# Kernel tuning notes

Hardware: AMD Instinct MI355X
Metric: run time of the kernel (lower is better)

## Reference

```python
import jax, jax.numpy as jnp
import numpy as np
from jax import lax

S, L = 8192, 16
N_WORD, N_CHAR = 50000, 128
WORD_DIM, CHAR_DIM = 256, 64
WORD_HID, CHAR_HID = 512, 128
N_TAG = 64


def _lstm_gates(x, h, Wih, Whh, bih, bhh):
    # x: [..., D], h: [..., H]; torch gate order: i, f, g, o
    g = x @ Wih.T + h @ Whh.T + bih + bhh
    i, f, gg, o = jnp.split(g, 4, axis=-1)
    return jax.nn.sigmoid(i), jax.nn.sigmoid(f), jnp.tanh(gg), jax.nn.sigmoid(o)


def setup_inputs() -> dict:
    key = jax.random.key(0)
    ks = jax.random.split(key, 16)
    sc = 0.1
    inp = {
        'x': jax.random.randint(ks[0], (S,), 0, N_WORD),
        'chars': jax.random.randint(ks[1], (S, L), 0, N_CHAR),
        'lengths': jax.random.randint(ks[2], (S,), 0, L),
        'word_emb': jax.random.normal(ks[3], (N_WORD, WORD_DIM), jnp.float32) * sc,
        'char_emb': jax.random.normal(ks[4], (N_CHAR, CHAR_DIM), jnp.float32) * sc,
        'c_Wih': jax.random.normal(ks[5], (4 * CHAR_HID, CHAR_DIM), jnp.float32) * sc,
        'c_Whh': jax.random.normal(ks[6], (4 * CHAR_HID, CHAR_HID), jnp.float32) * sc,
        'c_bih': jax.random.normal(ks[7], (4 * CHAR_HID,), jnp.float32) * sc,
        'c_bhh': jax.random.normal(ks[8], (4 * CHAR_HID,), jnp.float32) * sc,
        'w_Wih': jax.random.normal(ks[9], (4 * WORD_HID, WORD_DIM + CHAR_HID), jnp.float32) * sc,
        'w_Whh': jax.random.normal(ks[10], (4 * WORD_HID, WORD_HID), jnp.float32) * sc,
        'w_bih': jax.random.normal(ks[11], (4 * WORD_HID,), jnp.float32) * sc,
        'w_bhh': jax.random.normal(ks[12], (4 * WORD_HID,), jnp.float32) * sc,
        'lin_W': jax.random.normal(ks[13], (N_TAG, WORD_HID), jnp.float32) * sc,
        'lin_b': jax.random.normal(ks[14], (N_TAG,), jnp.float32) * sc,
    }
    return inp


def _char_features(chars, lengths, char_emb, Wih, Whh, bih, bhh):
    # batched char LSTM over all S words at once; returns final CELL state (h[1] in torch)
    emb = char_emb[chars]              # [S, L, char_dim]
    xs = jnp.swapaxes(emb, 0, 1)       # [L, S, char_dim]
    h0 = jnp.zeros((chars.shape[0], CHAR_HID), emb.dtype)
    c0 = jnp.zeros_like(h0)

    def step(carry, inp):
        h, c = carry
        x_t, t = inp
        i, f, g, o = _lstm_gates(x_t, h, Wih, Whh, bih, bhh)
        c_new = f * c + i * g
        h_new = o * jnp.tanh(c_new)
        m = (t < lengths)[:, None]     # only update within each word's true length
        return (jnp.where(m, h_new, h), jnp.where(m, c_new, c)), None

    (h, c), _ = lax.scan(step, (h0, c0), (xs, jnp.arange(L)))
    return c                            # [S, char_hidden]


def _word_lstm(seq, Wih, Whh, bih, bhh):
    # seq: [S, D] single sequence (batch=1 in original)
    h0 = jnp.zeros((WORD_HID,), seq.dtype)
    c0 = jnp.zeros_like(h0)

    def step(carry, x_t):
        h, c = carry
        i, f, g, o = _lstm_gates(x_t, h, Wih, Whh, bih, bhh)
        c = f * c + i * g
        h = o * jnp.tanh(c)
        return (h, c), h

    _, hs = lax.scan(step, (h0, c0), seq)
    return hs                           # [S, word_hidden]


def reference(x, chars, lengths, word_emb, char_emb,
              c_Wih, c_Whh, c_bih, c_bhh,
              w_Wih, w_Whh, w_bih, w_bhh,
              lin_W, lin_b):
    char_feat = _char_features(chars, lengths, char_emb, c_Wih, c_Whh, c_bih, c_bhh)
    we = word_emb[x]                                    # [S, word_dim]
    seq = jnp.concatenate([we, char_feat], axis=1)      # [S, word_dim+char_hidden]
    hs = _word_lstm(seq, w_Wih, w_Whh, w_bih, w_bhh)    # [S, word_hidden]
    logits = hs @ lin_W.T + lin_b                       # [S, n_tag]
    return jax.nn.log_softmax(logits, axis=1)
```

## Files before the change

kernel.cpp:

```cpp
#include <hip/hip_runtime.h>
#include <hip/hip_bf16.h>

#define S_LEN 8192
#define CLEN 16
#define WDIM 256
#define CDIM 64
#define CHID 128
#define WHID 512
#define GDIM 2048
#define NTAG 64
#define KDIM 384
#define NWG 32

typedef unsigned long long u64;

__device__ __forceinline__ float sigmoidf_(float x) {
  return 1.0f / (1.0f + __expf(-x));
}
__device__ __forceinline__ float tanhf_(float x) {
  return 1.0f - 2.0f / (__expf(2.0f * x) + 1.0f);
}

__global__ __launch_bounds__(256)
void char_lstm_kernel(const int* __restrict__ chars, const int* __restrict__ lengths,
                      const float* __restrict__ emb, const float* __restrict__ Wih,
                      const float* __restrict__ Whh, const float* __restrict__ bih,
                      const float* __restrict__ bhh, float* __restrict__ cf)
{
  __shared__ float xs[16][CDIM];
  __shared__ float hsm[16][CHID];
  __shared__ int cidx[16];
  __shared__ int lens[16];
  const int tid = threadIdx.x;
  const int grp = tid >> 7;
  const int j = tid & 127;
  const int wb = blockIdx.x * 16;

  for (int i = tid; i < 16 * CHID; i += 256) (&hsm[0][0])[i] = 0.f;
  if (tid < 16) lens[tid] = lengths[wb + tid];
  float c[8];
#pragma unroll
  for (int w = 0; w < 8; ++w) c[w] = 0.f;
  const float bi = bih[j] + bhh[j];
  const float bf = bih[CHID + j] + bhh[CHID + j];
  const float bg = bih[2 * CHID + j] + bhh[2 * CHID + j];
  const float bo = bih[3 * CHID + j] + bhh[3 * CHID + j];

  for (int t = 0; t < CLEN; ++t) {
    __syncthreads();
    if (tid < 16) cidx[tid] = chars[(wb + tid) * CLEN + t];
    __syncthreads();
    {
      int e = tid * 4;
      int wi = e >> 6;
      int k = e & 63;
      const float4 v = *(const float4*)(emb + (size_t)cidx[wi] * CDIM + k);
      *(float4*)(&xs[wi][k]) = v;
    }
    __syncthreads();
    float ai[8], af[8], ag[8], ao[8];
#pragma unroll
    for (int w = 0; w < 8; ++w) { ai[w] = bi; af[w] = bf; ag[w] = bg; ao[w] = bo; }
    for (int k = 0; k < CDIM; k += 4) {
      float4 w0 = *(const float4*)(Wih + (size_t)j * CDIM + k);
      float4 w1 = *(const float4*)(Wih + (size_t)(CHID + j) * CDIM + k);
      float4 w2 = *(const float4*)(Wih + (size_t)(2 * CHID + j) * CDIM + k);
      float4 w3 = *(const float4*)(Wih + (size_t)(3 * CHID + j) * CDIM + k);
#pragma unroll
      for (int s = 0; s < 4; ++s) {
        float wiv = (&w0.x)[s], wfv = (&w1.x)[s], wgv = (&w2.x)[s], wov = (&w3.x)[s];
#pragma unroll
        for (int w = 0; w < 8; ++w) {
          float xv = xs[grp * 8 + w][k + s];
          ai[w] = fmaf(wiv, xv, ai[w]);
          af[w] = fmaf(wfv, xv, af[w]);
          ag[w] = fmaf(wgv, xv, ag[w]);
          ao[w] = fmaf(wov, xv, ao[w]);
        }
      }
    }
    for (int k = 0; k < CHID; k += 4) {
      float4 w0 = *(const float4*)(Whh + (size_t)j * CHID + k);
      float4 w1 = *(const float4*)(Whh + (size_t)(CHID + j) * CHID + k);
      float4 w2 = *(const float4*)(Whh + (size_t)(2 * CHID + j) * CHID + k);
      float4 w3 = *(const float4*)(Whh + (size_t)(3 * CHID + j) * CHID + k);
#pragma unroll
      for (int s = 0; s < 4; ++s) {
        float wiv = (&w0.x)[s], wfv = (&w1.x)[s], wgv = (&w2.x)[s], wov = (&w3.x)[s];
#pragma unroll
        for (int w = 0; w < 8; ++w) {
          float hv = hsm[grp * 8 + w][k + s];
          ai[w] = fmaf(wiv, hv, ai[w]);
          af[w] = fmaf(wfv, hv, af[w]);
          ag[w] = fmaf(wgv, hv, ag[w]);
          ao[w] = fmaf(wov, hv, ao[w]);
        }
      }
    }
    __syncthreads();
#pragma unroll
    for (int w = 0; w < 8; ++w) {
      if (t < lens[grp * 8 + w]) {
        float iv = sigmoidf_(ai[w]);
        float fv = sigmoidf_(af[w]);
        float gv = tanhf_(ag[w]);
        float ov = sigmoidf_(ao[w]);
        c[w] = fv * c[w] + iv * gv;
        hsm[grp * 8 + w][j] = ov * tanhf_(c[w]);
      }
    }
  }
#pragma unroll
  for (int w = 0; w < 8; ++w)
    cf[(size_t)(wb + grp * 8 + w) * CHID + j] = c[w];
}

#define BM 64
#define BN 64
#define BK 32
__global__ __launch_bounds__(256)
void gx_gemm_kernel(const int* __restrict__ x, const float* __restrict__ word_emb,
                    const float* __restrict__ char_feat, const float* __restrict__ Wih,
                    const float* __restrict__ bih, const float* __restrict__ bhh,
                    float* __restrict__ Gx)
{
  __shared__ float As[BK][BM + 1];
  __shared__ float Bs[BK][BN + 1];
  __shared__ int xidx[BM];
  const int tid = threadIdx.x;
  const int tx = tid & 15, ty = tid >> 4;
  const int m0 = blockIdx.y * BM;
  const int n0 = blockIdx.x * BN;
  if (tid < BM) xidx[tid] = x[m0 + tid];
  float acc[4][4] = {};
  for (int k0 = 0; k0 < KDIM; k0 += BK) {
    __syncthreads();
    {
      int i = tid >> 5;
      int kk = tid & 31;
#pragma unroll
      for (int l = 0; l < 8; ++l) {
        int row = i + l * 8;
        int k = k0 + kk;
        int tt = m0 + row;
        float v = (k < WDIM) ? word_emb[(size_t)xidx[row] * WDIM + k]
                             : char_feat[(size_t)tt * CHID + (k - WDIM)];
        As[kk][row] = v;
      }
    }
    {
      int jjj = tid >> 5;
      int kk = tid & 31;
#pragma unroll
      for (int l = 0; l < 8; ++l) {
        int col = jjj + l * 8;
        Bs[kk][col] = Wih[(size_t)(n0 + col) * KDIM + k0 + kk];
      }
    }
    __syncthreads();
#pragma unroll
    for (int kk = 0; kk < BK; ++kk) {
      float a[4], b[4];
#pragma unroll
      for (int m = 0; m < 4; ++m) a[m] = As[kk][ty * 4 + m];
#pragma unroll
      for (int n = 0; n < 4; ++n) b[n] = Bs[kk][tx * 4 + n];
#pragma unroll
      for (int m = 0; m < 4; ++m)
#pragma unroll
        for (int n = 0; n < 4; ++n)
          acc[m][n] = fmaf(a[m], b[n], acc[m][n]);
    }
  }
#pragma unroll
  for (int n = 0; n < 4; ++n) {
    int g = n0 + tx * 4 + n;
    float bias = bih[g] + bhh[g];
#pragma unroll
    for (int m = 0; m < 4; ++m) {
      int tt = m0 + ty * 4 + m;
      Gx[(size_t)tt * GDIM + g] = acc[m][n] + bias;
    }
  }
}

__global__ __launch_bounds__(256, 1)
void word_lstm_seq(const float* __restrict__ Whh, const float* __restrict__ Gx,
                   float* __restrict__ hs, u64* hbuf)
{
  __shared__ float h_lds[WHID];
  __shared__ float red[2][256];
  const int tid = threadIdx.x;
  const int wg = blockIdx.x;
  const int cc = tid >> 6;
  const int lane = tid & 63;
  const int kb = cc * 128;

  const int grow = (lane >> 4) * WHID + wg * 16 + (lane & 15);
  float wl[128];
  {
    const float* wsrc = Whh + (size_t)grow * WHID + kb;
#pragma unroll
    for (int k = 0; k < 128; ++k) wl[k] = wsrc[k];
  }

  float c_state = 0.f;

  for (int t = 0; t < S_LEN; ++t) {
    float gxv = 0.f;
    if (tid < 64)
      gxv = Gx[(size_t)t * GDIM + grow];
    if (t > 0) {
      const u64* base = hbuf + (size_t)(t & 1) * WHID + kb;
      const int s0 = 2 * lane;
      u64 a, b;
      const unsigned want = (unsigned)t;
      while (true) {
        a = __hip_atomic_load(base + s0, __ATOMIC_RELAXED,
                              __HIP_MEMORY_SCOPE_AGENT);
        b = __hip_atomic_load(base + s0 + 1, __ATOMIC_RELAXED,
                              __HIP_MEMORY_SCOPE_AGENT);
        if ((unsigned)(a >> 32) == want && (unsigned)(b >> 32) == want) break;
      }
      float2 hv2 = make_float2(__uint_as_float((unsigned)a),
                               __uint_as_float((unsigned)b));
      *(float2*)(&h_lds[kb + s0]) = hv2;
    } else {
      *(float2*)(&h_lds[kb + 2 * lane]) = make_float2(0.f, 0.f);
    }
    __threadfence_block();
    float acc = 0.f;
#pragma unroll
    for (int g = 0; g < 32; ++g) {
      float4 hv = *(const float4*)(&h_lds[kb + 4 * g]);
      acc = fmaf(wl[4 * g + 0], hv.x, acc);
      acc = fmaf(wl[4 * g + 1], hv.y, acc);
      acc = fmaf(wl[4 * g + 2], hv.z, acc);
      acc = fmaf(wl[4 * g + 3], hv.w, acc);
    }
    red[t & 1][tid] = acc;
    __syncthreads();
    if (tid < 64) {
      const float* rp = &red[t & 1][0];
      float s = rp[tid] + rp[64 + tid] + rp[128 + tid] + rp[192 + tid] + gxv;
      float act = ((tid >> 4) == 2) ? tanhf_(s) : sigmoidf_(s);
      int jj = tid & 15;
      float iv = __shfl(act, jj);
      float fv = __shfl(act, 16 + jj);
      float gv = __shfl(act, 32 + jj);
      float ov = __shfl(act, 48 + jj);
      if (tid < 16) {
        c_state = fv * c_state + iv * gv;
        float hv = ov * tanhf_(c_state);
        const int hidx = wg * 16 + tid;
        u64 pkt = ((u64)(unsigned)(t + 1) << 32) | (u64)__float_as_uint(hv);
        (void)__hip_atomic_exchange(
            &hbuf[(size_t)((t + 1) & 1) * WHID + hidx], pkt,
            __ATOMIC_RELAXED, __HIP_MEMORY_SCOPE_AGENT);
        hs[(size_t)t * WHID + hidx] = hv;
      }
    }
  }
}

__global__ __launch_bounds__(256)
void tag_kernel(const float* __restrict__ hs, const float* __restrict__ W,
                const float* __restrict__ b, float* __restrict__ out)
{
  const int wave = threadIdx.x >> 6;
  const int lane = threadIdx.x & 63;
  const int t = blockIdx.x * 4 + wave;
  const float* hr = hs + (size_t)t * WHID;
  const float* wr = W + (size_t)lane * WHID;
  float acc = b[lane];
  for (int k = 0; k < WHID; k += 4) {
    float4 wv = *(const float4*)(wr + k);
    float4 hv = *(const float4*)(hr + k);
    acc = fmaf(wv.x, hv.x, acc);
    acc = fmaf(wv.y, hv.y, acc);
    acc = fmaf(wv.z, hv.z, acc);
    acc = fmaf(wv.w, hv.w, acc);
  }
  float m = acc;
#pragma unroll
  for (int off = 32; off > 0; off >>= 1) m = fmaxf(m, __shfl_xor(m, off));
  float e = __expf(acc - m);
  float sum = e;
#pragma unroll
  for (int off = 32; off > 0; off >>= 1) sum += __shfl_xor(sum, off);
  out[(size_t)t * NTAG + lane] = (acc - m) - __logf(sum);
}

extern "C" void kernel_launch(void* const* d_in, const int* in_sizes, int n_in,
                              void* d_out, int out_size, void* d_ws, size_t ws_size,
                              hipStream_t stream)
{
  const int* x          = (const int*)d_in[0];
  const int* chars      = (const int*)d_in[1];
  const int* lengths    = (const int*)d_in[2];
  const float* word_emb = (const float*)d_in[3];
  const float* char_emb = (const float*)d_in[4];
  const float* c_Wih    = (const float*)d_in[5];
  const float* c_Whh    = (const float*)d_in[6];
  const float* c_bih    = (const float*)d_in[7];
  const float* c_bhh    = (const float*)d_in[8];
  const float* w_Wih    = (const float*)d_in[9];
  const float* w_Whh    = (const float*)d_in[10];
  const float* w_bih    = (const float*)d_in[11];
  const float* w_bhh    = (const float*)d_in[12];
  const float* lin_W    = (const float*)d_in[13];
  const float* lin_b    = (const float*)d_in[14];
  float* out = (float*)d_out;

  char* ws = (char*)d_ws;
  u64*   hbuf      = (u64*)ws;
  float* char_feat = (float*)(ws + 8192);
  float* Gx        = (float*)(ws + 8192 + (size_t)S_LEN * CHID * 4);
  float* hs        = (float*)(ws + 8192 + (size_t)S_LEN * CHID * 4
                                        + (size_t)S_LEN * GDIM * 4);

  hipMemsetAsync(ws, 0, 8192, stream);

  char_lstm_kernel<<<S_LEN / 16, 256, 0, stream>>>(
      chars, lengths, char_emb, c_Wih, c_Whh, c_bih, c_bhh, char_feat);

  dim3 g2(GDIM / BN, S_LEN / BM);
  gx_gemm_kernel<<<g2, 256, 0, stream>>>(
      x, word_emb, char_feat, w_Wih, w_bih, w_bhh, Gx);

  word_lstm_seq<<<NWG, 256, 0, stream>>>(w_Whh, Gx, hs, hbuf);

  tag_kernel<<<S_LEN / 4, 256, 0, stream>>>(hs, lin_W, lin_b, out);
}
```

Before: 15.86 ms.

## Fuse char LSTM, input GEMM and word LSTM into one dataflow-synchronized kernel

Merges the char LSTM, the Gx input-projection GEMM and the sequential word LSTM into one persistent launch. Blocks are partitioned by role, and per-tile atomic counters signal readiness: a GEMM tile waits for its char-feature rows, and the word LSTM waits for each 64-step Gx tile. The serial recurrence can therefore start while the parallel stages are still running. This relies on the recurrence blocks (lowest block IDs) being co-resident and on forward progress of spinning blocks, and launch_bounds(256,1) now applies to every role, which may reduce occupancy for the char and GEMM blocks.

```diff
diff --git a/kernel.cpp b/kernel.cpp
--- a/kernel.cpp
+++ b/kernel.cpp
@@ -11,6 +11,9 @@
 #define NTAG 64
 #define KDIM 384
 #define NWG 32
+#define NCHAR_BLK 512
+#define NGEMM_BLK 4096
+#define GRID_TOTAL (NWG + NCHAR_BLK + NGEMM_BLK)
 
 typedef unsigned long long u64;
 
@@ -21,245 +24,267 @@
   return 1.0f - 2.0f / (__expf(2.0f * x) + 1.0f);
 }
 
-__global__ __launch_bounds__(256)
-void char_lstm_kernel(const int* __restrict__ chars, const int* __restrict__ lengths,
-                      const float* __restrict__ emb, const float* __restrict__ Wih,
-                      const float* __restrict__ Whh, const float* __restrict__ bih,
-                      const float* __restrict__ bhh, float* __restrict__ cf)
+__global__ __launch_bounds__(256, 1)
+void fused_kernel(const int* __restrict__ x, const int* __restrict__ chars,
+                  const int* __restrict__ lengths,
+                  const float* __restrict__ word_emb,
+                  const float* __restrict__ char_emb,
+                  const float* __restrict__ cWih, const float* __restrict__ cWhh,
+                  const float* __restrict__ cbih, const float* __restrict__ cbhh,
+                  const float* __restrict__ wWih, const float* __restrict__ wWhh,
+                  const float* __restrict__ wbih, const float* __restrict__ wbhh,
+                  float* __restrict__ char_feat, float* __restrict__ Gx,
+                  float* __restrict__ hs, u64* hbuf,
+                  int* cf_cnt, int* gx_cnt)
 {
-  __shared__ float xs[16][CDIM];
-  __shared__ float hsm[16][CHID];
-  __shared__ int cidx[16];
-  __shared__ int lens[16];
+  __shared__ __align__(16) char smem[17408];
   const int tid = threadIdx.x;
-  const int grp = tid >> 7;
-  const int j = tid & 127;
-  const int wb = blockIdx.x * 16;
-
-  for (int i = tid; i < 16 * CHID; i += 256) (&hsm[0][0])[i] = 0.f;
-  if (tid < 16) lens[tid] = lengths[wb + tid];
-  float c[8];
-#pragma unroll
-  for (int w = 0; w < 8; ++w) c[w] = 0.f;
-  const float bi = bih[j] + bhh[j];
-  const float bf = bih[CHID + j] + bhh[CHID + j];
-  const float bg = bih[2 * CHID + j] + bhh[2 * CHID + j];
-  const float bo = bih[3 * CHID + j] + bhh[3 * CHID + j];
-
-  for (int t = 0; t < CLEN; ++t) {
+  const int bid = blockIdx.x;
+
+  if (bid < NWG) {
+    float* h_lds = (float*)smem;
+    float(*red)[256] = (float(*)[256])(smem + 2048);
+    const int wg = bid;
+    const int cc = tid >> 6;
+    const int lane = tid & 63;
+    const int kb = cc * 128;
+    const int grow = (lane >> 4) * WHID + wg * 16 + (lane & 15);
+
+    const int growL = (lane >> 4) * WHID + wg * 16 + (lane & 15);
+    float wl[128];
+    {
+      const float* wsrc = wWhh + (size_t)growL * WHID + kb;
+#pragma unroll
+      for (int k = 0; k < 128; ++k) wl[k] = wsrc[k];
+    }
+
+    float c_state = 0.f;
+
+    for (int t = 0; t < S_LEN; ++t) {
+      const int par = t & 1;
+      float gxv = 0.f;
+      if (tid < 64) {
+        if ((t & 63) == 0) {
+          const int mt = t >> 6;
+          while (__hip_atomic_load(&gx_cnt[mt], __ATOMIC_ACQUIRE,
+                                   __HIP_MEMORY_SCOPE_AGENT) < 32) {}
+        }
+        gxv = Gx[(size_t)t * GDIM + grow];
+      }
+      float v0 = 0.f, v1 = 0.f;
+      if (t > 0) {
+        const u64* ps = hbuf + (size_t)par * WHID + kb + 2 * lane;
+        const unsigned want = (unsigned)t;
+        u64 a, b;
+        do {
+          a = __hip_atomic_load(ps + 0, __ATOMIC_RELAXED, __HIP_MEMORY_SCOPE_AGENT);
+          b = __hip_atomic_load(ps + 1, __ATOMIC_RELAXED, __HIP_MEMORY_SCOPE_AGENT);
+        } while (((unsigned)(a >> 32) != want) | ((unsigned)(b >> 32) != want));
+        v0 = __uint_as_float((unsigned)a);
+        v1 = __uint_as_float((unsigned)b);
+      }
+      *(float2*)(&h_lds[kb + 2 * lane]) = make_float2(v0, v1);
+      __threadfence_block();
+      float acc = 0.f;
+#pragma unroll
+      for (int g = 0; g < 32; ++g) {
+        float4 hv = *(const float4*)(&h_lds[kb + 4 * g]);
+        acc = fmaf(wl[4 * g + 0], hv.x, acc);
+        acc = fmaf(wl[4 * g + 1], hv.y, acc);
+        acc = fmaf(wl[4 * g + 2], hv.z, acc);
+        acc = fmaf(wl[4 * g + 3], hv.w, acc);
+      }
+      red[par][tid] = acc;
+      __syncthreads();
+      if (tid < 64) {
+        const float* rp = red[par];
+        float s = rp[tid] + rp[64 + tid] + rp[128 + tid] + rp[192 + tid] + gxv;
+        float act = ((tid >> 4) == 2) ? tanhf_(s) : sigmoidf_(s);
+        int jj = tid & 15;
+        float iv = __shfl(act, jj);
+        float fv = __shfl(act, 16 + jj);
+        float gv = __shfl(act, 32 + jj);
+        float ov = __shfl(act, 48 + jj);
+        if (tid < 16) {
+          c_state = fv * c_state + iv * gv;
+          float hv = ov * tanhf_(c_state);
+          const int hidx = wg * 16 + tid;
+          const u64 pkt =
+              ((u64)(unsigned)(t + 1) << 32) | (u64)__float_as_uint(hv);
+          (void)__hip_atomic_exchange(
+              &hbuf[(size_t)((t + 1) & 1) * WHID + hidx], pkt,
+              __ATOMIC_RELAXED, __HIP_MEMORY_SCOPE_AGENT);
+          hs[(size_t)t * WHID + hidx] = hv;
+        }
+      }
+    }
+
+  } else if (bid < NWG + NCHAR_BLK) {
+    float(*xs)[CDIM] = (float(*)[CDIM])smem;
+    float(*hsm)[CHID] = (float(*)[CHID])(smem + 4096);
+    int* cidx = (int*)(smem + 12288);
+    int* lens = (int*)(smem + 12352);
+    const int grp = tid >> 7;
+    const int j = tid & 127;
+    const int cb = bid - NWG;
+    const int wb = cb * 16;
+
+    for (int i = tid; i < 16 * CHID; i += 256) (&hsm[0][0])[i] = 0.f;
+    if (tid < 16) lens[tid] = lengths[wb + tid];
+    float c[8];
+#pragma unroll
+    for (int w = 0; w < 8; ++w) c[w] = 0.f;
+    const float bi = cbih[j] + cbhh[j];
+    const float bf = cbih[CHID + j] + cbhh[CHID + j];
+    const float bg = cbih[2 * CHID + j] + cbhh[2 * CHID + j];
+    const float bo = cbih[3 * CHID + j] + cbhh[3 * CHID + j];
+
+    for (int t = 0; t < CLEN; ++t) {
+      __syncthreads();
+      if (tid < 16) cidx[tid] = chars[(wb + tid) * CLEN + t];
+      __syncthreads();
+      {
+        int e = tid * 4;
+        int wi = e >> 6;
+        int k = e & 63;
+        const float4 v = *(const float4*)(char_emb + (size_t)cidx[wi] * CDIM + k);
+        *(float4*)(&xs[wi][k]) = v;
+      }
+      __syncthreads();
+      float ai[8], af[8], ag[8], ao[8];
+#pragma unroll
+      for (int w = 0; w < 8; ++w) { ai[w] = bi; af[w] = bf; ag[w] = bg; ao[w] = bo; }
+      for (int k = 0; k < CDIM; k += 4) {
+        float4 w0 = *(const float4*)(cWih + (size_t)j * CDIM + k);
+        float4 w1 = *(const float4*)(cWih + (size_t)(CHID + j) * CDIM + k);
+        float4 w2 = *(const float4*)(cWih + (size_t)(2 * CHID + j) * CDIM + k);
+        float4 w3 = *(const float4*)(cWih + (size_t)(3 * CHID + j) * CDIM + k);
+#pragma unroll
+        for (int s = 0; s < 4; ++s) {
+          float wiv = (&w0.x)[s], wfv = (&w1.x)[s], wgv = (&w2.x)[s], wov = (&w3.x)[s];
+#pragma unroll
+          for (int w = 0; w < 8; ++w) {
+            float xv = xs[grp * 8 + w][k + s];
+            ai[w] = fmaf(wiv, xv, ai[w]);
+            af[w] = fmaf(wfv, xv, af[w]);
+            ag[w] = fmaf(wgv, xv, ag[w]);
+            ao[w] = fmaf(wov, xv, ao[w]);
+          }
+        }
+      }
+      for (int k = 0; k < CHID; k += 4) {
+        float4 w0 = *(const float4*)(cWhh + (size_t)j * CHID + k);
+        float4 w1 = *(const float4*)(cWhh + (size_t)(CHID + j) * CHID + k);
+        float4 w2 = *(const float4*)(cWhh + (size_t)(2 * CHID + j) * CHID + k);
+        float4 w3 = *(const float4*)(cWhh + (size_t)(3 * CHID + j) * CHID + k);
+#pragma unroll
+        for (int s = 0; s < 4; ++s) {
+          float wiv = (&w0.x)[s], wfv = (&w1.x)[s], wgv = (&w2.x)[s], wov = (&w3.x)[s];
+#pragma unroll
+          for (int w = 0; w < 8; ++w) {
+            float hv = hsm[grp * 8 + w][k + s];
+            ai[w] = fmaf(wiv, hv, ai[w]);
+            af[w] = fmaf(wfv, hv, af[w]);
+            ag[w] = fmaf(wgv, hv, ag[w]);
+            ao[w] = fmaf(wov, hv, ao[w]);
+          }
+        }
+      }
+      __syncthreads();
+#pragma unroll
+      for (int w = 0; w < 8; ++w) {
+        if (t < lens[grp * 8 + w]) {
+          float iv = sigmoidf_(ai[w]);
+          float fv = sigmoidf_(af[w]);
+          float gv = tanhf_(ag[w]);
+          float ov = sigmoidf_(ao[w]);
+          c[w] = fv * c[w] + iv * gv;
+          hsm[grp * 8 + w][j] = ov * tanhf_(c[w]);
+        }
+      }
+    }
+#pragma unroll
+    for (int w = 0; w < 8; ++w)
+      char_feat[(size_t)(wb + grp * 8 + w) * CHID + j] = c[w];
+    __threadfence();
     __syncthreads();
-    if (tid < 16) cidx[tid] = chars[(wb + tid) * CLEN + t];
+    if (tid == 0)
+      (void)__hip_atomic_fetch_add(&cf_cnt[cb >> 2], 1, __ATOMIC_RELEASE,
+                                   __HIP_MEMORY_SCOPE_AGENT);
+
+  } else {
+    float(*As)[65] = (float(*)[65])smem;
+    float(*Bs)[65] = (float(*)[65])(smem + 8320);
+    int* xidx = (int*)(smem + 16640);
+    const int bid2 = bid - NWG - NCHAR_BLK;
+    const int m = bid2 >> 5;
+    const int n = bid2 & 31;
+    const int m0 = m * 64;
+    const int n0 = n * 64;
+    const int tx = tid & 15, ty = tid >> 4;
+
+    if (tid == 0) {
+      while (__hip_atomic_load(&cf_cnt[m], __ATOMIC_ACQUIRE,
+                               __HIP_MEMORY_SCOPE_AGENT) < 4) {}
+    }
     __syncthreads();
-    {
-      int e = tid * 4;
-      int wi = e >> 6;
-      int k = e & 63;
-      const float4 v = *(const float4*)(emb + (size_t)cidx[wi] * CDIM + k);
-      *(float4*)(&xs[wi][k]) = v;
-    }
+    if (tid < 64) xidx[tid] = x[m0 + tid];
+
+    float acc[4][4] = {};
+    for (int k0 = 0; k0 < KDIM; k0 += 32) {
+      __syncthreads();
+      {
+        int i = tid >> 5;
+        int kk = tid & 31;
+#pragma unroll
+        for (int l = 0; l < 8; ++l) {
+          int row = i + l * 8;
+          int k = k0 + kk;
+          int tt = m0 + row;
+          float v = (k < WDIM) ? word_emb[(size_t)xidx[row] * WDIM + k]
+                               : char_feat[(size_t)tt * CHID + (k - WDIM)];
+          As[kk][row] = v;
+        }
+      }
+      {
+        int jjj = tid >> 5;
+        int kk = tid & 31;
+#pragma unroll
+        for (int l = 0; l < 8; ++l) {
+          int col = jjj + l * 8;
+          Bs[kk][col] = wWih[(size_t)(n0 + col) * KDIM + k0 + kk];
+        }
+      }
+      __syncthreads();
+#pragma unroll
+      for (int kk = 0; kk < 32; ++kk) {
+        float a[4], b[4];
+#pragma unroll
+        for (int mm = 0; mm < 4; ++mm) a[mm] = As[kk][ty * 4 + mm];
+#pragma unroll
+        for (int nn = 0; nn < 4; ++nn) b[nn] = Bs[kk][tx * 4 + nn];
+#pragma unroll
+        for (int mm = 0; mm < 4; ++mm)
+#pragma unroll
+          for (int nn = 0; nn < 4; ++nn)
+            acc[mm][nn] = fmaf(a[mm], b[nn], acc[mm][nn]);
+      }
+    }
+#pragma unroll
+    for (int nn = 0; nn < 4; ++nn) {
+      int g = n0 + tx * 4 + nn;
+      float bias = wbih[g] + wbhh[g];
+#pragma unroll
+      for (int mm = 0; mm < 4; ++mm) {
+        int tt = m0 + ty * 4 + mm;
+        Gx[(size_t)tt * GDIM + g] = acc[mm][nn] + bias;
+      }
+    }
+    __threadfence();
     __syncthreads();
-    float ai[8], af[8], ag[8], ao[8];
-#pragma unroll
-    for (int w = 0; w < 8; ++w) { ai[w] = bi; af[w] = bf; ag[w] = bg; ao[w] = bo; }
-    for (int k = 0; k < CDIM; k += 4) {
-      float4 w0 = *(const float4*)(Wih + (size_t)j * CDIM + k);
-      float4 w1 = *(const float4*)(Wih + (size_t)(CHID + j) * CDIM + k);
-      float4 w2 = *(const float4*)(Wih + (size_t)(2 * CHID + j) * CDIM + k);
-      float4 w3 = *(const float4*)(Wih + (size_t)(3 * CHID + j) * CDIM + k);
-#pragma unroll
-      for (int s = 0; s < 4; ++s) {
-        float wiv = (&w0.x)[s], wfv = (&w1.x)[s], wgv = (&w2.x)[s], wov = (&w3.x)[s];
-#pragma unroll
-        for (int w = 0; w < 8; ++w) {
-          float xv = xs[grp * 8 + w][k + s];
-          ai[w] = fmaf(wiv, xv, ai[w]);
-          af[w] = fmaf(wfv, xv, af[w]);
-          ag[w] = fmaf(wgv, xv, ag[w]);
-          ao[w] = fmaf(wov, xv, ao[w]);
-        }
-      }
-    }
-    for (int k = 0; k < CHID; k += 4) {
-      float4 w0 = *(const float4*)(Whh + (size_t)j * CHID + k);
-      float4 w1 = *(const float4*)(Whh + (size_t)(CHID + j) * CHID + k);
-      float4 w2 = *(const float4*)(Whh + (size_t)(2 * CHID + j) * CHID + k);
-      float4 w3 = *(const float4*)(Whh + (size_t)(3 * CHID + j) * CHID + k);
-#pragma unroll
-      for (int s = 0; s < 4; ++s) {
-        float wiv = (&w0.x)[s], wfv = (&w1.x)[s], wgv = (&w2.x)[s], wov = (&w3.x)[s];
-#pragma unroll
-        for (int w = 0; w < 8; ++w) {
-          float hv = hsm[grp * 8 + w][k + s];
-          ai[w] = fmaf(wiv, hv, ai[w]);
-          af[w] = fmaf(wfv, hv, af[w]);
-          ag[w] = fmaf(wgv, hv, ag[w]);
-          ao[w] = fmaf(wov, hv, ao[w]);
-        }
-      }
-    }
-    __syncthreads();
-#pragma unroll
-    for (int w = 0; w < 8; ++w) {
-      if (t < lens[grp * 8 + w]) {
-        float iv = sigmoidf_(ai[w]);
-        float fv = sigmoidf_(af[w]);
-        float gv = tanhf_(ag[w]);
-        float ov = sigmoidf_(ao[w]);
-        c[w] = fv * c[w] + iv * gv;
-        hsm[grp * 8 + w][j] = ov * tanhf_(c[w]);
-      }
-    }
-  }
-#pragma unroll
-  for (int w = 0; w < 8; ++w)
-    cf[(size_t)(wb + grp * 8 + w) * CHID + j] = c[w];
-}
-
-#define BM 64
-#define BN 64
-#define BK 32
-__global__ __launch_bounds__(256)
-void gx_gemm_kernel(const int* __restrict__ x, const float* __restrict__ word_emb,
-                    const float* __restrict__ char_feat, const float* __restrict__ Wih,
-                    const float* __restrict__ bih, const float* __restrict__ bhh,
-                    float* __restrict__ Gx)
-{
-  __shared__ float As[BK][BM + 1];
-  __shared__ float Bs[BK][BN + 1];
-  __shared__ int xidx[BM];
-  const int tid = threadIdx.x;
-  const int tx = tid & 15, ty = tid >> 4;
-  const int m0 = blockIdx.y * BM;
-  const int n0 = blockIdx.x * BN;
-  if (tid < BM) xidx[tid] = x[m0 + tid];
-  float acc[4][4] = {};
-  for (int k0 = 0; k0 < KDIM; k0 += BK) {
-    __syncthreads();
-    {
-      int i = tid >> 5;
-      int kk = tid & 31;
-#pragma unroll
-      for (int l = 0; l < 8; ++l) {
-        int row = i + l * 8;
-        int k = k0 + kk;
-        int tt = m0 + row;
-        float v = (k < WDIM) ? word_emb[(size_t)xidx[row] * WDIM + k]
-                             : char_feat[(size_t)tt * CHID + (k - WDIM)];
-        As[kk][row] = v;
-      }
-    }
-    {
-      int jjj = tid >> 5;
-      int kk = tid & 31;
-#pragma unroll
-      for (int l = 0; l < 8; ++l) {
-        int col = jjj + l * 8;
-        Bs[kk][col] = Wih[(size_t)(n0 + col) * KDIM + k0 + kk];
-      }
-    }
-    __syncthreads();
-#pragma unroll
-    for (int kk = 0; kk < BK; ++kk) {
-      float a[4], b[4];
-#pragma unroll
-      for (int m = 0; m < 4; ++m) a[m] = As[kk][ty * 4 + m];
-#pragma unroll
-      for (int n = 0; n < 4; ++n) b[n] = Bs[kk][tx * 4 + n];
-#pragma unroll
-      for (int m = 0; m < 4; ++m)
-#pragma unroll
-        for (int n = 0; n < 4; ++n)
-          acc[m][n] = fmaf(a[m], b[n], acc[m][n]);
-    }
-  }
-#pragma unroll
-  for (int n = 0; n < 4; ++n) {
-    int g = n0 + tx * 4 + n;
-    float bias = bih[g] + bhh[g];
-#pragma unroll
-    for (int m = 0; m < 4; ++m) {
-      int tt = m0 + ty * 4 + m;
-      Gx[(size_t)tt * GDIM + g] = acc[m][n] + bias;
-    }
-  }
-}
-
-__global__ __launch_bounds__(256, 1)
-void word_lstm_seq(const float* __restrict__ Whh, const float* __restrict__ Gx,
-                   float* __restrict__ hs, u64* hbuf)
-{
-  __shared__ float h_lds[WHID];
-  __shared__ float red[2][256];
-  const int tid = threadIdx.x;
-  const int wg = blockIdx.x;
-  const int cc = tid >> 6;
-  const int lane = tid & 63;
-  const int kb = cc * 128;
-
-  const int grow = (lane >> 4) * WHID + wg * 16 + (lane & 15);
-  float wl[128];
-  {
-    const float* wsrc = Whh + (size_t)grow * WHID + kb;
-#pragma unroll
-    for (int k = 0; k < 128; ++k) wl[k] = wsrc[k];
-  }
-
-  float c_state = 0.f;
-
-  for (int t = 0; t < S_LEN; ++t) {
-    float gxv = 0.f;
-    if (tid < 64)
-      gxv = Gx[(size_t)t * GDIM + grow];
-    if (t > 0) {
-      const u64* base = hbuf + (size_t)(t & 1) * WHID + kb;
-      const int s0 = 2 * lane;
-      u64 a, b;
-      const unsigned want = (unsigned)t;
-      while (true) {
-        a = __hip_atomic_load(base + s0, __ATOMIC_RELAXED,
-                              __HIP_MEMORY_SCOPE_AGENT);
-        b = __hip_atomic_load(base + s0 + 1, __ATOMIC_RELAXED,
-                              __HIP_MEMORY_SCOPE_AGENT);
-        if ((unsigned)(a >> 32) == want && (unsigned)(b >> 32) == want) break;
-      }
-      float2 hv2 = make_float2(__uint_as_float((unsigned)a),
-                               __uint_as_float((unsigned)b));
-      *(float2*)(&h_lds[kb + s0]) = hv2;
-    } else {
-      *(float2*)(&h_lds[kb + 2 * lane]) = make_float2(0.f, 0.f);
-    }
-    __threadfence_block();
-    float acc = 0.f;
-#pragma unroll
-    for (int g = 0; g < 32; ++g) {
-      float4 hv = *(const float4*)(&h_lds[kb + 4 * g]);
-      acc = fmaf(wl[4 * g + 0], hv.x, acc);
-      acc = fmaf(wl[4 * g + 1], hv.y, acc);
-      acc = fmaf(wl[4 * g + 2], hv.z, acc);
-      acc = fmaf(wl[4 * g + 3], hv.w, acc);
-    }
-    red[t & 1][tid] = acc;
-    __syncthreads();
-    if (tid < 64) {
-      const float* rp = &red[t & 1][0];
-      float s = rp[tid] + rp[64 + tid] + rp[128 + tid] + rp[192 + tid] + gxv;
-      float act = ((tid >> 4) == 2) ? tanhf_(s) : sigmoidf_(s);
-      int jj = tid & 15;
-      float iv = __shfl(act, jj);
-      float fv = __shfl(act, 16 + jj);
-      float gv = __shfl(act, 32 + jj);
-      float ov = __shfl(act, 48 + jj);
-      if (tid < 16) {
-        c_state = fv * c_state + iv * gv;
-        float hv = ov * tanhf_(c_state);
-        const int hidx = wg * 16 + tid;
-        u64 pkt = ((u64)(unsigned)(t + 1) << 32) | (u64)__float_as_uint(hv);
-        (void)__hip_atomic_exchange(
-            &hbuf[(size_t)((t + 1) & 1) * WHID + hidx], pkt,
-            __ATOMIC_RELAXED, __HIP_MEMORY_SCOPE_AGENT);
-        hs[(size_t)t * WHID + hidx] = hv;
-      }
-    }
+    if (tid == 0)
+      (void)__hip_atomic_fetch_add(&gx_cnt[m], 1, __ATOMIC_RELEASE,
+                                   __HIP_MEMORY_SCOPE_AGENT);
   }
 }
 
@@ -314,21 +339,20 @@
 
   char* ws = (char*)d_ws;
   u64*   hbuf      = (u64*)ws;
-  float* char_feat = (float*)(ws + 8192);
-  float* Gx        = (float*)(ws + 8192 + (size_t)S_LEN * CHID * 4);
-  float* hs        = (float*)(ws + 8192 + (size_t)S_LEN * CHID * 4
-                                        + (size_t)S_LEN * GDIM * 4);
-
-  hipMemsetAsync(ws, 0, 8192, stream);
-
-  char_lstm_kernel<<<S_LEN / 16, 256, 0, stream>>>(
-      chars, lengths, char_emb, c_Wih, c_Whh, c_bih, c_bhh, char_feat);
-
-  dim3 g2(GDIM / BN, S_LEN / BM);
-  gx_gemm_kernel<<<g2, 256, 0, stream>>>(
-      x, word_emb, char_feat, w_Wih, w_bih, w_bhh, Gx);
-
-  word_lstm_seq<<<NWG, 256, 0, stream>>>(w_Whh, Gx, hs, hbuf);
+  int*   cf_cnt    = (int*)(ws + 8192);
+  int*   gx_cnt    = (int*)(ws + 8704);
+  float* char_feat = (float*)(ws + 12288);
+  float* Gx        = (float*)(ws + 12288 + (size_t)S_LEN * CHID * 4);
+  float* hs        = (float*)(ws + 12288 + (size_t)S_LEN * CHID * 4
+                                         + (size_t)S_LEN * GDIM * 4);
+
+  hipMemsetAsync(ws, 0, 12288, stream);
+
+  fused_kernel<<<GRID_TOTAL, 256, 0, stream>>>(
+      x, chars, lengths, word_emb, char_emb,
+      c_Wih, c_Whh, c_bih, c_bhh,
+      w_Wih, w_Whh, w_bih, w_bhh,
+      char_feat, Gx, hs, hbuf, cf_cnt, gx_cnt);
 
   tag_kernel<<<S_LEN / 4, 256, 0, stream>>>(hs, lin_W, lin_b, out);
 }
```

Measured after the change: 18.22 ms. 14.9% more time.
